# Performance work log

Hardware: AMD Instinct MI355X
Metric: run time of the kernel (lower is better)

## Reference

```python
import jax, jax.numpy as jnp
import numpy as np

NUM_HEADS = 32
NUM_KV_HEADS = 8
HEAD_DIM = 128
SCALING = 0.08838834764831845  # 1/sqrt(128)
B, T = 2, 2048


def setup_inputs() -> dict:
    key = jax.random.key(0)
    kq, kk, kv = jax.random.split(key, 3)
    q = jax.random.normal(kq, (B, T, NUM_HEADS, HEAD_DIM), dtype=jnp.float32)
    k = jax.random.normal(kk, (B, T, NUM_KV_HEADS, HEAD_DIM), dtype=jnp.float32)
    v = jax.random.normal(kv, (B, T, NUM_KV_HEADS, HEAD_DIM), dtype=jnp.float32)
    return {"q": q, "k": k, "v": v}


def _attn(q, k, v):
    # GQA expand: [B,T,nKv,D] -> [B,T,nH,D]
    n_rep = NUM_HEADS // NUM_KV_HEADS
    Bq, Tq = q.shape[0], q.shape[1]
    k = jnp.broadcast_to(k[:, :, :, None, :], (Bq, Tq, NUM_KV_HEADS, n_rep, HEAD_DIM)).reshape(Bq, Tq, NUM_HEADS, HEAD_DIM)
    v = jnp.broadcast_to(v[:, :, :, None, :], (Bq, Tq, NUM_KV_HEADS, n_rep, HEAD_DIM)).reshape(Bq, Tq, NUM_HEADS, HEAD_DIM)
    # scores: [B,H,T,T]
    scores = jnp.einsum('bqhd,bkhd->bhqk', q, k) * SCALING
    causal = jnp.triu(jnp.ones((Tq, Tq), dtype=bool), k=1)  # True above diagonal
    scores = jnp.where(causal, jnp.finfo(scores.dtype).min, scores)
    probs = jax.nn.softmax(scores, axis=-1)
    out = jnp.einsum('bhqk,bkhd->bqhd', probs, v)
    return out.reshape(Bq, Tq, NUM_HEADS * HEAD_DIM)


def reference(q, k, v):
    return _attn(q, k, v)
```

## Files before the change

### kernel.cpp

```cpp
#include <hip/hip_runtime.h>
#include <stdint.h>


typedef __attribute__((ext_vector_type(8))) __bf16 bf16x8;
typedef __attribute__((ext_vector_type(16))) float f32x16;

#define QSCALE (0.08838834764831845f * 1.4426950408889634f)

__global__ __launch_bounds__(256) void cvt_k(const float* __restrict__ k,
                                             unsigned short* __restrict__ kb) {
    unsigned tid = blockIdx.x * 256u + threadIdx.x;
    unsigned s = tid & 15u;
    unsigned h = (tid >> 4) & 7u;
    unsigned t = (tid >> 7) & 2047u;
    unsigned b = tid >> 18;
    const float4* src = (const float4*)(k + (size_t)tid * 8u);
    float4 f0 = src[0], f1 = src[1];
    bf16x8 r;
    r[0] = (__bf16)f0.x; r[1] = (__bf16)f0.y; r[2] = (__bf16)f0.z; r[3] = (__bf16)f0.w;
    r[4] = (__bf16)f1.x; r[5] = (__bf16)f1.y; r[6] = (__bf16)f1.z; r[7] = (__bf16)f1.w;
    size_t o = ((size_t)((b * 8u + h) * 2048u + t) * 16u + (s ^ (t & 7u))) * 8u;
    *(bf16x8*)(kb + o) = r;
}

__global__ __launch_bounds__(256) void cvt_v(const float* __restrict__ v,
                                             unsigned short* __restrict__ vtb) {
    unsigned tid = blockIdx.x * 256u + threadIdx.x;
    unsigned d = tid & 127u;
    unsigned oct = (tid >> 7) & 3u;
    unsigned tile = (tid >> 9) & 63u;
    unsigned kvh = (tid >> 15) & 7u;
    unsigned b = tid >> 18;
    const float* src = v + ((size_t)(b * 2048u + tile * 32u + oct * 8u) * 8u + kvh) * 128u + d;
    bf16x8 r;
#pragma unroll
    for (int e = 0; e < 8; ++e) r[e] = (__bf16)src[(size_t)e * 1024u];
    unsigned p = d >> 1;
    unsigned slot = (d & 1u) * 4u + oct;
    size_t off = (size_t)(b * 8u + kvh) * 262144u + (size_t)tile * 4096u
               + (p * 8u + (slot ^ (p & 7u))) * 8u;
    *(bf16x8*)(vtb + off) = r;
}

__device__ inline void load16_lds(const void* g, void* l) {
    __builtin_amdgcn_global_load_lds(
        (__attribute__((address_space(1))) void*)(g),
        (__attribute__((address_space(3))) void*)(l), 16, 0, 0);
}

union BW2 { unsigned u; __bf16 h[2]; };
union BW8 { unsigned u[4]; bf16x8 v; };

__global__ __launch_bounds__(256, 3) void attn_fwd(const float* __restrict__ qg,
                                                   const unsigned short* __restrict__ kb,
                                                   const unsigned short* __restrict__ vtb,
                                                   float* __restrict__ outg) {
    __shared__ __align__(16) unsigned short K0[32 * 128], K1[32 * 128], K2[32 * 128];
    __shared__ __align__(16) unsigned short V0[64 * 64],  V1[64 * 64],  V2[64 * 64];

    int bid = blockIdx.x;
    int kvh = bid & 7;
    int pos = bid >> 3;
    int qt = 15 - (pos >> 3);
    int sub = pos & 7;
    int b = sub & 1;
    int h = kvh * 4 + (sub >> 1);

    int tid = threadIdx.x;
    int lane = tid & 63;
    int w = tid >> 6;
    int lq = lane & 31;
    int hi = lane >> 5;
    bool bhi = (hi != 0);
    int q0w = qt * 128 + w * 32;
    int nt = 4 * (qt + 1);

    const unsigned short* kT = kb + (size_t)(b * 8 + kvh) * 262144u;
    const unsigned short* vT = vtb + (size_t)(b * 8 + kvh) * 262144u;

    auto stage = [&](int t, unsigned short* kd, unsigned short* vd) {
        const char* ks = (const char*)(kT + (size_t)t * 4096u);
        const char* vs = (const char*)(vT + (size_t)t * 4096u);
#pragma unroll
        for (int i = 0; i < 2; ++i) {
            load16_lds(ks + (i * 256 + tid) * 16, kd + (i * 256 + tid) * 8);
            load16_lds(vs + (i * 256 + tid) * 16, vd + (i * 256 + tid) * 8);
        }
    };

    stage(0, K0, V0);
    stage(1, K1, V1);

    bf16x8 qf[8];
    {
        const float* qp = qg + ((size_t)(b * 2048 + q0w + lq) * 32u + h) * 128u;
#pragma unroll
        for (int c = 0; c < 8; ++c) {
            int d0 = c * 16 + hi * 8;
            float4 f0 = *(const float4*)(qp + d0);
            float4 f1 = *(const float4*)(qp + d0 + 4);
            qf[c][0] = (__bf16)(f0.x * QSCALE); qf[c][1] = (__bf16)(f0.y * QSCALE);
            qf[c][2] = (__bf16)(f0.z * QSCALE); qf[c][3] = (__bf16)(f0.w * QSCALE);
            qf[c][4] = (__bf16)(f1.x * QSCALE); qf[c][5] = (__bf16)(f1.y * QSCALE);
            qf[c][6] = (__bf16)(f1.z * QSCALE); qf[c][7] = (__bf16)(f1.w * QSCALE);
        }
    }

    f32x16 acc[4];
#pragma unroll
    for (int dt = 0; dt < 4; ++dt)
#pragma unroll
        for (int r = 0; r < 16; ++r) acc[dt][r] = 0.f;
    float lrun = 0.f;

    unsigned short *kc = K0, *kn = K1, *kx = K2;
    unsigned short *vc = V0, *vn = V1, *vx = V2;

    for (int t = 0; t < nt; ++t) {
        asm volatile("s_waitcnt vmcnt(4)" ::: "memory");
        __builtin_amdgcn_s_barrier();
        if (t + 2 < nt) stage(t + 2, kx, vx);
        int kv0 = t * 32;
        if (kv0 <= q0w + 31) {
            f32x16 st0;
#pragma unroll
            for (int r = 0; r < 16; ++r) st0[r] = 0.f;
            __builtin_amdgcn_s_setprio(1);
#pragma unroll
            for (int c = 0; c < 8; ++c) {
                bf16x8 kf = *(const bf16x8*)&kc[lq * 128 + (((2 * c + hi) ^ (lq & 7)) << 3)];
                st0 = __builtin_amdgcn_mfma_f32_32x32x16_bf16(kf, qf[c], st0, 0, 0, 0);
            }
            __builtin_amdgcn_s_setprio(0);
            if (kv0 == q0w) {
#pragma unroll
                for (int r = 0; r < 16; ++r) {
                    int kvl = (r & 3) + 8 * (r >> 2) + 4 * hi;
                    if (kvl > lq) st0[r] = -1e30f;
                }
            }
#pragma unroll
            for (int r = 0; r < 16; ++r) st0[r] = exp2f(st0[r]);
            unsigned wv[8];
#pragma unroll
            for (int i = 0; i < 8; ++i) {
                BW2 t2; t2.h[0] = (__bf16)st0[2 * i]; t2.h[1] = (__bf16)st0[2 * i + 1];
                wv[i] = t2.u;
            }
            unsigned u0 = bhi ? wv[0] : wv[2]; u0 = __shfl_xor(u0, 32);
            unsigned u1 = bhi ? wv[1] : wv[3]; u1 = __shfl_xor(u1, 32);
            unsigned u2 = bhi ? wv[4] : wv[6]; u2 = __shfl_xor(u2, 32);
            unsigned u3 = bhi ? wv[5] : wv[7]; u3 = __shfl_xor(u3, 32);
            BW8 pb0, pb1;
            pb0.u[0] = bhi ? u0 : wv[0]; pb0.u[1] = bhi ? u1 : wv[1];
            pb0.u[2] = bhi ? wv[2] : u0; pb0.u[3] = bhi ? wv[3] : u1;
            pb1.u[0] = bhi ? u2 : wv[4]; pb1.u[1] = bhi ? u3 : wv[5];
            pb1.u[2] = bhi ? wv[6] : u2; pb1.u[3] = bhi ? wv[7] : u3;
            __builtin_amdgcn_s_setprio(1);
#pragma unroll
            for (int dt = 0; dt < 4; ++dt) {
                int drow = dt * 32 + lq;
                int pp = drow >> 1;
                int s0 = (drow & 1) * 4 + hi;
                int s1 = s0 + 2;
                bf16x8 vf0 = *(const bf16x8*)&vc[pp * 64 + ((s0 ^ (pp & 7)) << 3)];
                acc[dt] = __builtin_amdgcn_mfma_f32_32x32x16_bf16(vf0, pb0.v, acc[dt], 0, 0, 0);
                bf16x8 vf1 = *(const bf16x8*)&vc[pp * 64 + ((s1 ^ (pp & 7)) << 3)];
                acc[dt] = __builtin_amdgcn_mfma_f32_32x32x16_bf16(vf1, pb1.v, acc[dt], 0, 0, 0);
            }
            __builtin_amdgcn_s_setprio(0);
            float s8[8];
#pragma unroll
            for (int i = 0; i < 8; ++i) s8[i] = st0[2 * i] + st0[2 * i + 1];
#pragma unroll
            for (int i = 0; i < 4; ++i) s8[i] = s8[i] + s8[i + 4];
            float ps = (s8[0] + s8[1]) + (s8[2] + s8[3]);
            ps += __shfl_xor(ps, 32);
            lrun += ps;
        }
        unsigned short* tk = kc; kc = kn; kn = kx; kx = tk;
        unsigned short* tv = vc; vc = vn; vn = vx; vx = tv;
    }

    float il = 1.0f / lrun;
    float* ob = outg + ((size_t)(b * 2048 + q0w + lq) * 32u + h) * 128u;
#pragma unroll
    for (int dt = 0; dt < 4; ++dt)
#pragma unroll
        for (int rq = 0; rq < 4; ++rq) {
            int d = dt * 32 + rq * 8 + hi * 4;
            float4 o4 = { acc[dt][rq * 4 + 0] * il, acc[dt][rq * 4 + 1] * il,
                          acc[dt][rq * 4 + 2] * il, acc[dt][rq * 4 + 3] * il };
            *(float4*)(ob + d) = o4;
        }
}

extern "C" void kernel_launch(void* const* d_in, const int* in_sizes, int n_in,
                              void* d_out, int out_size, void* d_ws, size_t ws_size,
                              hipStream_t stream) {
    const float* q = (const float*)d_in[0];
    const float* k = (const float*)d_in[1];
    const float* v = (const float*)d_in[2];
    float* out = (float*)d_out;
    unsigned short* kbuf = (unsigned short*)d_ws;
    unsigned short* vbuf = kbuf + (size_t)2 * 8 * 2048 * 128;
    cvt_k<<<2048, 256, 0, stream>>>(k, kbuf);
    cvt_v<<<2048, 256, 0, stream>>>(v, vbuf);
    attn_fwd<<<1024, 256, 0, stream>>>(q, kbuf, vbuf, out);
}
```

Measured before the change: 117.8 us.

## Software-pipeline QK^T and PV across iterations with four-stage LDS ring

```diff
diff --git a/kernel.cpp b/kernel.cpp
--- a/kernel.cpp
+++ b/kernel.cpp
@@ -55,8 +55,8 @@
                                                    const unsigned short* __restrict__ kb,
                                                    const unsigned short* __restrict__ vtb,
                                                    float* __restrict__ outg) {
-    __shared__ __align__(16) unsigned short K0[32 * 128], K1[32 * 128], K2[32 * 128];
-    __shared__ __align__(16) unsigned short V0[64 * 64],  V1[64 * 64],  V2[64 * 64];
+    __shared__ __align__(16) unsigned short K0[32*128], K1[32*128], K2[32*128], K3[32*128];
+    __shared__ __align__(16) unsigned short V0[64*64],  V1[64*64],  V2[64*64],  V3[64*64];
 
     int bid = blockIdx.x;
     int kvh = bid & 7;
@@ -68,11 +68,10 @@
 
     int tid = threadIdx.x;
     int lane = tid & 63;
-    int w = tid >> 6;
     int lq = lane & 31;
     int hi = lane >> 5;
     bool bhi = (hi != 0);
-    int q0w = qt * 128 + w * 32;
+    int q0w = qt * 128 + (tid >> 6) * 32;
     int nt = 4 * (qt + 1);
 
     const unsigned short* kT = kb + (size_t)(b * 8 + kvh) * 262144u;
@@ -112,76 +111,88 @@
 #pragma unroll
         for (int r = 0; r < 16; ++r) acc[dt][r] = 0.f;
     float lrun = 0.f;
-
-    unsigned short *kc = K0, *kn = K1, *kx = K2;
-    unsigned short *vc = V0, *vn = V1, *vx = V2;
-
-    for (int t = 0; t < nt; ++t) {
-        asm volatile("s_waitcnt vmcnt(4)" ::: "memory");
-        __builtin_amdgcn_s_barrier();
-        if (t + 2 < nt) stage(t + 2, kx, vx);
-        int kv0 = t * 32;
-        if (kv0 <= q0w + 31) {
-            f32x16 st0;
-#pragma unroll
-            for (int r = 0; r < 16; ++r) st0[r] = 0.f;
-            __builtin_amdgcn_s_setprio(1);
-#pragma unroll
-            for (int c = 0; c < 8; ++c) {
-                bf16x8 kf = *(const bf16x8*)&kc[lq * 128 + (((2 * c + hi) ^ (lq & 7)) << 3)];
-                st0 = __builtin_amdgcn_mfma_f32_32x32x16_bf16(kf, qf[c], st0, 0, 0, 0);
-            }
-            __builtin_amdgcn_s_setprio(0);
-            if (kv0 == q0w) {
-#pragma unroll
-                for (int r = 0; r < 16; ++r) {
-                    int kvl = (r & 3) + 8 * (r >> 2) + 4 * hi;
-                    if (kvl > lq) st0[r] = -1e30f;
-                }
-            }
-#pragma unroll
-            for (int r = 0; r < 16; ++r) st0[r] = exp2f(st0[r]);
-            unsigned wv[8];
-#pragma unroll
-            for (int i = 0; i < 8; ++i) {
-                BW2 t2; t2.h[0] = (__bf16)st0[2 * i]; t2.h[1] = (__bf16)st0[2 * i + 1];
-                wv[i] = t2.u;
-            }
-            unsigned u0 = bhi ? wv[0] : wv[2]; u0 = __shfl_xor(u0, 32);
-            unsigned u1 = bhi ? wv[1] : wv[3]; u1 = __shfl_xor(u1, 32);
-            unsigned u2 = bhi ? wv[4] : wv[6]; u2 = __shfl_xor(u2, 32);
-            unsigned u3 = bhi ? wv[5] : wv[7]; u3 = __shfl_xor(u3, 32);
-            BW8 pb0, pb1;
-            pb0.u[0] = bhi ? u0 : wv[0]; pb0.u[1] = bhi ? u1 : wv[1];
-            pb0.u[2] = bhi ? wv[2] : u0; pb0.u[3] = bhi ? wv[3] : u1;
-            pb1.u[0] = bhi ? u2 : wv[4]; pb1.u[1] = bhi ? u3 : wv[5];
-            pb1.u[2] = bhi ? wv[6] : u2; pb1.u[3] = bhi ? wv[7] : u3;
-            __builtin_amdgcn_s_setprio(1);
-#pragma unroll
-            for (int dt = 0; dt < 4; ++dt) {
-                int drow = dt * 32 + lq;
-                int pp = drow >> 1;
-                int s0 = (drow & 1) * 4 + hi;
-                int s1 = s0 + 2;
-                bf16x8 vf0 = *(const bf16x8*)&vc[pp * 64 + ((s0 ^ (pp & 7)) << 3)];
-                acc[dt] = __builtin_amdgcn_mfma_f32_32x32x16_bf16(vf0, pb0.v, acc[dt], 0, 0, 0);
-                bf16x8 vf1 = *(const bf16x8*)&vc[pp * 64 + ((s1 ^ (pp & 7)) << 3)];
-                acc[dt] = __builtin_amdgcn_mfma_f32_32x32x16_bf16(vf1, pb1.v, acc[dt], 0, 0, 0);
-            }
-            __builtin_amdgcn_s_setprio(0);
-            float s8[8];
-#pragma unroll
-            for (int i = 0; i < 8; ++i) s8[i] = st0[2 * i] + st0[2 * i + 1];
-#pragma unroll
-            for (int i = 0; i < 4; ++i) s8[i] = s8[i] + s8[i + 4];
-            float ps = (s8[0] + s8[1]) + (s8[2] + s8[3]);
-            ps += __shfl_xor(ps, 32);
-            lrun += ps;
-        }
-        unsigned short* tk = kc; kc = kn; kn = kx; kx = tk;
-        unsigned short* tv = vc; vc = vn; vn = vx; vx = tv;
+    f32x16 stA, stB;
+
+#define ITER(T, CUR, PRV, KC, VP, KS, VS)                                        \
+    do {                                                                          \
+        int t_ = (T);                                                             \
+        if (t_ + 2 < nt) { asm volatile("s_waitcnt vmcnt(4)" ::: "memory"); }     \
+        else             { asm volatile("s_waitcnt vmcnt(0)" ::: "memory"); }     \
+        __builtin_amdgcn_s_barrier();                                             \
+        if (t_ + 2 < nt) stage(t_ + 2, KS, VS);                                   \
+        int kv0_ = t_ * 32;                                                       \
+        if (kv0_ <= q0w + 31) {                                 \
+            _Pragma("unroll")                                                     \
+            for (int r = 0; r < 16; ++r) CUR[r] = 0.f;                            \
+            __builtin_amdgcn_s_setprio(1);                                        \
+            _Pragma("unroll")                                                     \
+            for (int c = 0; c < 8; ++c) {                                         \
+                bf16x8 kf = *(const bf16x8*)&KC[lq * 128 +                        \
+                                (((2 * c + hi) ^ (lq & 7)) << 3)];                \
+                CUR = __builtin_amdgcn_mfma_f32_32x32x16_bf16(kf, qf[c], CUR,     \
+                                                              0, 0, 0);           \
+            }                                                                     \
+            __builtin_amdgcn_s_setprio(0);                                        \
+            if (kv0_ == q0w) {                                 \
+                _Pragma("unroll")                                                 \
+                for (int r = 0; r < 16; ++r) {                                    \
+                    int kvl = (r & 3) + 8 * (r >> 2) + 4 * hi;                    \
+                    if (kvl > lq) CUR[r] = -1e30f;                                \
+                }                                                                 \
+            }                                                                     \
+        }                                                                         \
+        if (t_ >= 1 && kv0_ - 32 <= q0w + 31) {              \
+            _Pragma("unroll")                                                     \
+            for (int r = 0; r < 16; ++r) PRV[r] = exp2f(PRV[r]);                  \
+            unsigned wv[8];                                                       \
+            _Pragma("unroll")                                                     \
+            for (int i = 0; i < 8; ++i) {                                         \
+                BW2 t2; t2.h[0] = (__bf16)PRV[2*i]; t2.h[1] = (__bf16)PRV[2*i+1]; \
+                wv[i] = t2.u;                                                     \
+            }                                                                     \
+            unsigned u0 = bhi ? wv[0] : wv[2]; u0 = __shfl_xor(u0, 32);           \
+            unsigned u1 = bhi ? wv[1] : wv[3]; u1 = __shfl_xor(u1, 32);           \
+            unsigned u2 = bhi ? wv[4] : wv[6]; u2 = __shfl_xor(u2, 32);           \
+            unsigned u3 = bhi ? wv[5] : wv[7]; u3 = __shfl_xor(u3, 32);           \
+            BW8 pb0, pb1;                                                         \
+            pb0.u[0] = bhi ? u0 : wv[0]; pb0.u[1] = bhi ? u1 : wv[1];             \
+            pb0.u[2] = bhi ? wv[2] : u0; pb0.u[3] = bhi ? wv[3] : u1;             \
+            pb1.u[0] = bhi ? u2 : wv[4]; pb1.u[1] = bhi ? u3 : wv[5];             \
+            pb1.u[2] = bhi ? wv[6] : u2; pb1.u[3] = bhi ? wv[7] : u3;             \
+            __builtin_amdgcn_s_setprio(1);                                        \
+            _Pragma("unroll")                                                     \
+            for (int dt = 0; dt < 4; ++dt) {                                      \
+                int drow = dt * 32 + lq;                                          \
+                int pp = drow >> 1;                                               \
+                int s0 = (drow & 1) * 4 + hi;                                     \
+                bf16x8 vf0 = *(const bf16x8*)&VP[pp * 64 + ((s0 ^ (pp & 7)) << 3)];\
+                acc[dt] = __builtin_amdgcn_mfma_f32_32x32x16_bf16(vf0, pb0.v,     \
+                                                                  acc[dt], 0,0,0);\
+                bf16x8 vf1 = *(const bf16x8*)&VP[pp * 64 +                        \
+                                               (((s0 + 2) ^ (pp & 7)) << 3)];     \
+                acc[dt] = __builtin_amdgcn_mfma_f32_32x32x16_bf16(vf1, pb1.v,     \
+                                                                  acc[dt], 0,0,0);\
+            }                                                                     \
+            __builtin_amdgcn_s_setprio(0);                                        \
+            float s8[8];                                                          \
+            _Pragma("unroll")                                                     \
+            for (int i = 0; i < 8; ++i) s8[i] = PRV[2*i] + PRV[2*i+1];            \
+            _Pragma("unroll")                                                     \
+            for (int i = 0; i < 4; ++i) s8[i] = s8[i] + s8[i + 4];                \
+            lrun += (s8[0] + s8[1]) + (s8[2] + s8[3]);                            \
+        }                                                                         \
+    } while (0)
+
+    for (int t = 0; t < nt; t += 4) {
+        ITER(t + 0, stA, stB, K0, V3, K2, V2);
+        ITER(t + 1, stB, stA, K1, V0, K3, V3);
+        ITER(t + 2, stA, stB, K2, V1, K0, V0);
+        ITER(t + 3, stB, stA, K3, V2, K1, V1);
     }
-
+    ITER(nt, stA, stB, K0, V3, K0, V0);
+#undef ITER
+
+    lrun += __shfl_xor(lrun, 32);
     float il = 1.0f / lrun;
     float* ob = outg + ((size_t)(b * 2048 + q0w + lq) * 32u + h) * 128u;
 #pragma unroll
```

Measured after the change: 134.6 us. 14.3% more time.

## Permute K rows within tiles to drop cross-lane shuffles building P operand

Applied to the files above, without the earlier changes.

```diff
diff --git a/kernel.cpp b/kernel.cpp
--- a/kernel.cpp
+++ b/kernel.cpp
@@ -6,6 +6,11 @@
 typedef __attribute__((ext_vector_type(16))) float f32x16;
 
 #define QSCALE (0.08838834764831845f * 1.4426950408889634f)
+
+__host__ __device__ inline unsigned pi32(unsigned x) {
+    unsigned q2 = (x >> 2) & 3u;
+    return (q2 == 1u || q2 == 2u) ? (x ^ 12u) : x;
+}
 
 __global__ __launch_bounds__(256) void cvt_k(const float* __restrict__ k,
                                              unsigned short* __restrict__ kb) {
@@ -19,7 +24,8 @@
     bf16x8 r;
     r[0] = (__bf16)f0.x; r[1] = (__bf16)f0.y; r[2] = (__bf16)f0.z; r[3] = (__bf16)f0.w;
     r[4] = (__bf16)f1.x; r[5] = (__bf16)f1.y; r[6] = (__bf16)f1.z; r[7] = (__bf16)f1.w;
-    size_t o = ((size_t)((b * 8u + h) * 2048u + t) * 16u + (s ^ (t & 7u))) * 8u;
+    unsigned tp = (t & ~31u) | pi32(t & 31u);
+    size_t o = ((size_t)((b * 8u + h) * 2048u + tp) * 16u + (s ^ (tp & 7u))) * 8u;
     *(bf16x8*)(kb + o) = r;
 }
 
@@ -68,11 +74,9 @@
 
     int tid = threadIdx.x;
     int lane = tid & 63;
-    int w = tid >> 6;
     int lq = lane & 31;
     int hi = lane >> 5;
-    bool bhi = (hi != 0);
-    int q0w = qt * 128 + w * 32;
+    int q0w = qt * 128 + (tid >> 6) * 32;
     int nt = 4 * (qt + 1);
 
     const unsigned short* kT = kb + (size_t)(b * 8 + kvh) * 262144u;
@@ -117,7 +121,8 @@
     unsigned short *vc = V0, *vn = V1, *vx = V2;
 
     for (int t = 0; t < nt; ++t) {
-        asm volatile("s_waitcnt vmcnt(4)" ::: "memory");
+        if (t + 2 < nt) { asm volatile("s_waitcnt vmcnt(4)" ::: "memory"); }
+        else            { asm volatile("s_waitcnt vmcnt(0)" ::: "memory"); }
         __builtin_amdgcn_s_barrier();
         if (t + 2 < nt) stage(t + 2, kx, vx);
         int kv0 = t * 32;
@@ -136,26 +141,20 @@
 #pragma unroll
                 for (int r = 0; r < 16; ++r) {
                     int kvl = (r & 3) + 8 * (r >> 2) + 4 * hi;
-                    if (kvl > lq) st0[r] = -1e30f;
+                    int q2 = (kvl >> 2) & 3;
+                    int kva = (q2 == 1 || q2 == 2) ? (kvl ^ 12) : kvl;
+                    if (kva > lq) st0[r] = -1e30f;
                 }
             }
 #pragma unroll
             for (int r = 0; r < 16; ++r) st0[r] = exp2f(st0[r]);
-            unsigned wv[8];
-#pragma unroll
-            for (int i = 0; i < 8; ++i) {
-                BW2 t2; t2.h[0] = (__bf16)st0[2 * i]; t2.h[1] = (__bf16)st0[2 * i + 1];
-                wv[i] = t2.u;
-            }
-            unsigned u0 = bhi ? wv[0] : wv[2]; u0 = __shfl_xor(u0, 32);
-            unsigned u1 = bhi ? wv[1] : wv[3]; u1 = __shfl_xor(u1, 32);
-            unsigned u2 = bhi ? wv[4] : wv[6]; u2 = __shfl_xor(u2, 32);
-            unsigned u3 = bhi ? wv[5] : wv[7]; u3 = __shfl_xor(u3, 32);
             BW8 pb0, pb1;
-            pb0.u[0] = bhi ? u0 : wv[0]; pb0.u[1] = bhi ? u1 : wv[1];
-            pb0.u[2] = bhi ? wv[2] : u0; pb0.u[3] = bhi ? wv[3] : u1;
-            pb1.u[0] = bhi ? u2 : wv[4]; pb1.u[1] = bhi ? u3 : wv[5];
-            pb1.u[2] = bhi ? wv[6] : u2; pb1.u[3] = bhi ? wv[7] : u3;
+#pragma unroll
+            for (int i = 0; i < 4; ++i) {
+                BW2 a; a.h[0] = (__bf16)st0[2 * i];     a.h[1] = (__bf16)st0[2 * i + 1];
+                BW2 c; c.h[0] = (__bf16)st0[8 + 2 * i]; c.h[1] = (__bf16)st0[9 + 2 * i];
+                pb0.u[i] = a.u; pb1.u[i] = c.u;
+            }
             __builtin_amdgcn_s_setprio(1);
 #pragma unroll
             for (int dt = 0; dt < 4; ++dt) {
@@ -174,14 +173,13 @@
             for (int i = 0; i < 8; ++i) s8[i] = st0[2 * i] + st0[2 * i + 1];
 #pragma unroll
             for (int i = 0; i < 4; ++i) s8[i] = s8[i] + s8[i + 4];
-            float ps = (s8[0] + s8[1]) + (s8[2] + s8[3]);
-            ps += __shfl_xor(ps, 32);
-            lrun += ps;
+            lrun += (s8[0] + s8[1]) + (s8[2] + s8[3]);
         }
         unsigned short* tk = kc; kc = kn; kn = kx; kx = tk;
         unsigned short* tv = vc; vc = vn; vn = vx; vx = tv;
     }
 
+    lrun += __shfl_xor(lrun, 32);
     float il = 1.0f / lrun;
     float* ob = outg + ((size_t)(b * 2048 + q0w + lq) * 32u + h) * 128u;
 #pragma unroll
```

Result: faster. 110.4 us (-6.3%).
